# Kernel tuning notes

Hardware: AMD Instinct MI355X
Metric: run time of the kernel (lower is better)

Reference implementation:

```python
import jax, jax.numpy as jnp
import numpy as np

B, T, N = 256, 4096, 64


def setup_inputs() -> dict:
    key = jax.random.key(0)
    u = jax.random.normal(key, (B, T), dtype=jnp.float32)
    # LRU-style stable parameterization: rho chosen so r = exp(-softplus(rho)) = radii
    radii = np.clip(0.9 + 0.0015 * np.arange(N), 1e-6, 1 - 1e-6)
    rho = np.log(np.expm1(-np.log(radii))).astype(np.float32)
    theta = (np.pi * np.arange(N) / N).astype(np.float32)
    return {
        "u": u,
        "rho": jnp.asarray(rho),
        "theta": jnp.asarray(theta),
        "b_real": jnp.ones((N,), jnp.float32),
        "b_imag": jnp.zeros((N,), jnp.float32),
        "c_real": jnp.ones((N,), jnp.float32),
        "c_imag": jnp.zeros((N,), jnp.float32),
    }


def reference(u, rho, theta, b_real, b_imag, c_real, c_imag):
    # lambda = exp(-softplus(rho)) * exp(i*theta), strictly inside unit circle
    r = jnp.exp(-jax.nn.softplus(rho))
    lam = (r.astype(jnp.complex64) * jnp.exp(1j * theta)).astype(jnp.complex64)
    b = (b_real + 1j * b_imag).astype(jnp.complex64)
    c_conj = jnp.conj((c_real + 1j * c_imag).astype(jnp.complex64))
    # precompute driving term b * u_t for all t: (T, B, N)
    bu = jnp.swapaxes(b[None, None, :] * u[:, :, None], 0, 1)

    def step(x, bu_t):
        x = lam * x + bu_t            # (B, N) complex diagonal recurrence
        y_t = jnp.real(x @ c_conj)    # (B,) readout Re(c^H x)
        return x, y_t

    x0 = jnp.zeros((u.shape[0], rho.shape[0]), dtype=jnp.complex64)
    _, ys = jax.lax.scan(step, x0, bu)  # ys: (T, B)
    return jnp.swapaxes(ys, 0, 1)       # (B, T) float32
```

## Files before the change

### kernel.cpp

```cpp
#include <hip/hip_runtime.h>
#include <hip/hip_bf16.h>

#define T_LEN  4096
#define NLAG   5
#define CMAX   575
#define ESTR   728
#define ROUNDS 9

typedef __attribute__((ext_vector_type(8))) short short8;
typedef __attribute__((ext_vector_type(4))) float f32x4;

static __device__ __forceinline__ unsigned short f2bf(float f) {
  __hip_bfloat16 h = __float2bfloat16(f);
  return *reinterpret_cast<unsigned short*>(&h);
}

template <int CTRL>
static __device__ __forceinline__ float dppmov(float x) {
  return __int_as_float(__builtin_amdgcn_update_dpp(
      0, __float_as_int(x), CTRL, 0xF, 0xF, true));
}

#define CVT8(dst, va, vb) {                                                       \
    short8 _v;                                                                    \
    _v[0] = (short)f2bf((va).x); _v[1] = (short)f2bf((va).y);                     \
    _v[2] = (short)f2bf((va).z); _v[3] = (short)f2bf((va).w);                     \
    _v[4] = (short)f2bf((vb).x); _v[5] = (short)f2bf((vb).y);                     \
    _v[6] = (short)f2bf((vb).z); _v[7] = (short)f2bf((vb).w);                     \
    *reinterpret_cast<short8*>(dst) = _v; }

#define LBAR() { asm volatile("s_waitcnt lgkmcnt(0)" ::: "memory");               \
                 __builtin_amdgcn_s_barrier(); }

__global__ __launch_bounds__(512) void ssm_one(
    const float* __restrict__ u, const float* __restrict__ rho,
    const float* __restrict__ theta, const float* __restrict__ br,
    const float* __restrict__ bi, const float* __restrict__ cr,
    const float* __restrict__ ci, float* __restrict__ out) {
  __shared__ __align__(16) unsigned short Ab[2][8192];
  __shared__ __align__(16) unsigned short E8[8 * ESTR];

  const int tid = threadIdx.x;
  const int lane = tid & 63;
  const int w = tid >> 6;
  const bool prod = (w >= 4);
  const int pt = tid & 255;

  const int bid = blockIdx.x;
  const int swz = (bid & 7) * 32 + (bid >> 3);
  const int t0 = (swz & 63) * 64;
  const int b0 = (swz >> 6) * 64;

  const int lrow = lane >> 4, lc16 = lane & 15;
  const float4 z4 = make_float4(0.f, 0.f, 0.f, 0.f);
  float4 av[2][4][2];
  f32x4 acc[2][2] = {};

#define ISSUEA(j, S) { _Pragma("unroll") for (int h_ = 0; h_ < 4; ++h_) {         \
    const int hh = pt + 256 * h_;                                                 \
    const int r_ = hh >> 4, cg = hh & 15;                                         \
    const int gg = t0 - (j) * 128 + cg * 8;                                       \
    if ((unsigned)gg < 4096u) {                                                   \
      const float* p_ = u + (size_t)(b0 + r_) * T_LEN + gg;                       \
      av[S][h_][0] = *reinterpret_cast<const float4*>(p_);                        \
      av[S][h_][1] = *reinterpret_cast<const float4*>(p_ + 4);                    \
    } else { av[S][h_][0] = z4; av[S][h_][1] = z4; } } }

#define WRITEA(buf, S) { _Pragma("unroll") for (int h_ = 0; h_ < 4; ++h_) {       \
    const int hh = pt + 256 * h_;                                                 \
    const int r_ = hh >> 4, cg = hh & 15;                                         \
    const int eo = r_ * 128 + ((cg * 8) ^ ((r_ & 7) << 3));                       \
    CVT8(&Ab[buf][eo], av[S][h_][0], av[S][h_][1]); } }

  if (prod) ISSUEA(0, 0);

  {
    const short8 z8 = {};
    for (int c = tid; c < ESTR; c += 512)
      *reinterpret_cast<short8*>(&E8[c * 8]) = z8;
  }

  const float rh = rho[lane], th = theta[lane];
  const float lr2 = -1.4426950408f * log1pf(expf(rh));
  const float rr_ = exp2f(lr2);
  const float lre = rr_ * __cosf(th), lim = rr_ * __sinf(th);
  const float brv = br[lane], biv = bi[lane];
  const float crv = cr[lane], civ = ci[lane];
  const float wre = crv * brv + civ * biv;
  const float wim = crv * biv - civ * brv;

  float Lr[9], Li[9];
  Lr[0] = 1.f; Li[0] = 0.f;
#pragma unroll
  for (int i = 1; i <= 8; ++i) {
    Lr[i] = Lr[i - 1] * lre - Li[i - 1] * lim;
    Li[i] = Lr[i - 1] * lim + Li[i - 1] * lre;
  }

  const float d0f = (float)(8 * ROUNDS * w);
  const float rd0 = exp2f(d0f * lr2);
  float f0 = d0f * (th * 0.15915494309f);
  f0 -= floorf(f0);
  const float a0 = 6.2831853072f * f0;
  const float c0 = __cosf(a0), s0 = __sinf(a0);
  float gr = rd0 * (wre * c0 - wim * s0);
  float gi = rd0 * (wre * s0 + wim * c0);

  const bool l0 = lane & 1, l1 = lane & 2, l3 = lane & 8;
  const int sig = ((lane & 1) << 2) | (lane & 2) | ((lane >> 3) & 1);
  const int cc  = ((lane >> 2) & 1) | ((lane >> 3) & 2) | ((lane >> 3) & 4);

  LBAR();

  for (int rnd = 0; rnd < ROUNDS; ++rnd) {
    float v[8];
#pragma unroll
    for (int i2 = 0; i2 < 8; ++i2)
      v[i2] = gr * Lr[i2] - gi * Li[i2];
    { const float ngr = gr * Lr[8] - gi * Li[8];
      const float ngi = gr * Li[8] + gi * Lr[8];
      gr = ngr; gi = ngi; }
    float s4[4];
#pragma unroll
    for (int i = 0; i < 4; ++i) {
      const float t = l0 ? v[i + 4] : v[i];
      const float u2 = l0 ? v[i] : v[i + 4];
      s4[i] = t + dppmov<0xB1>(u2);
    }
    float s2[2];
#pragma unroll
    for (int i = 0; i < 2; ++i) {
      const float t = l1 ? s4[i + 2] : s4[i];
      const float u2 = l1 ? s4[i] : s4[i + 2];
      s2[i] = t + dppmov<0x4E>(u2);
    }
    float y;
    { const float t = l3 ? s2[1] : s2[0];
      const float u2 = l3 ? s2[0] : s2[1];
      y = t + dppmov<0x128>(u2); }
    y += __shfl_xor(y, 4);
    y += __shfl_xor(y, 16);
    y += __shfl_xor(y, 32);
    const int d = 72 * w + 8 * rnd + sig;
    const int yy = CMAX - d;
    if (yy >= cc) E8[cc * ESTR + (yy - cc)] = f2bf(y);
  }

  if (prod) { WRITEA(0, 0); ISSUEA(1, 1); }
  LBAR();

#define COMPUTE(jj, buf) {                                                        \
    const unsigned short* A = Ab[buf];                                            \
    const int wm = w >> 1, wn = w & 1;                                            \
    const int pB = 7 - (lc16 & 7);                                                \
    _Pragma("unroll") for (int ks = 0; ks < 4; ++ks) {                            \
      short8 af[2], bfr[2];                                                       \
      _Pragma("unroll") for (int ft = 0; ft < 2; ++ft) {                          \
        const int r = wm * 32 + ft * 16 + lc16;                                   \
        const int pe = (ks * 32 + lrow * 8) ^ ((r & 7) << 3);                     \
        af[ft] = *reinterpret_cast<const short8*>(&A[r * 128 + pe]); }            \
      _Pragma("unroll") for (int fn = 0; fn < 2; ++fn) {                          \
        const int rB = wn * 32 + fn * 16 + lc16;                                  \
        const int x0 = CMAX - (jj) * 128 - rB + ks * 32 + lrow * 8 - pB;          \
        bfr[fn] = *reinterpret_cast<const short8*>(&E8[pB * ESTR + x0]); }        \
      _Pragma("unroll") for (int ft = 0; ft < 2; ++ft)                            \
        _Pragma("unroll") for (int fn = 0; fn < 2; ++fn)                          \
          acc[ft][fn] = __builtin_amdgcn_mfma_f32_16x16x32_bf16(                  \
              af[ft], bfr[fn], acc[ft][fn], 0, 0, 0); } }

#pragma unroll
  for (int j = 0; j < NLAG; ++j) {
    if (prod) {
      if (j + 1 < NLAG) WRITEA((j + 1) & 1, (j + 1) & 1);
      if (j + 2 < NLAG) ISSUEA(j + 2, j & 1);
    } else {
      COMPUTE(j, j & 1);
    }
    if (j < NLAG - 1) LBAR();
  }

  if (!prod) {
    const int wm = w >> 1, wn = w & 1;
#pragma unroll
    for (int ft = 0; ft < 2; ++ft)
#pragma unroll
      for (int fn = 0; fn < 2; ++fn)
#pragma unroll
        for (int rg = 0; rg < 4; ++rg) {
          const int row = b0 + wm * 32 + ft * 16 + lrow * 4 + rg;
          const int col = t0 + wn * 32 + fn * 16 + lc16;
          out[(size_t)row * T_LEN + col] = acc[ft][fn][rg];
        }
  }
#undef ISSUEA
#undef WRITEA
#undef COMPUTE
}

extern "C" void kernel_launch(void* const* d_in, const int* in_sizes, int n_in,
                              void* d_out, int out_size, void* d_ws, size_t ws_size,
                              hipStream_t stream) {
  const float* u     = (const float*)d_in[0];
  const float* rho   = (const float*)d_in[1];
  const float* theta = (const float*)d_in[2];
  const float* br    = (const float*)d_in[3];
  const float* bi    = (const float*)d_in[4];
  const float* cr    = (const float*)d_in[5];
  const float* ci    = (const float*)d_in[6];
  float* out = (float*)d_out;

  ssm_one<<<256, 512, 0, stream>>>(u, rho, theta, br, bi, cr, ci, out);
}
```

Measured before the change: 12.99 us.

## Double block to 1024 threads with split-K consumers and dedicated producer waves

The block grows from 512 to 1024 threads. Eight producer waves now share the global load of the input tile, each doing half as many loads per thread. Eight consumer waves split the MFMA K-loop in half, and the two partial accumulators are summed through a new LDS scratch buffer before the output store. The impulse-response table is now computed only by consumer waves while producers zero the table and issue the first load. This aims to cut per-wave serial work and latency in a short, latency-bound kernel. In exchange it adds a reduction barrier, extra LDS, and tighter register limits from the new launch bounds.

```diff
diff --git a/kernel.cpp b/kernel.cpp
--- a/kernel.cpp
+++ b/kernel.cpp
@@ -32,19 +32,20 @@
 #define LBAR() { asm volatile("s_waitcnt lgkmcnt(0)" ::: "memory");               \
                  __builtin_amdgcn_s_barrier(); }
 
-__global__ __launch_bounds__(512) void ssm_one(
+__global__ __launch_bounds__(1024, 4) void ssm_one(
     const float* __restrict__ u, const float* __restrict__ rho,
     const float* __restrict__ theta, const float* __restrict__ br,
     const float* __restrict__ bi, const float* __restrict__ cr,
     const float* __restrict__ ci, float* __restrict__ out) {
   __shared__ __align__(16) unsigned short Ab[2][8192];
   __shared__ __align__(16) unsigned short E8[8 * ESTR];
+  __shared__ __align__(16) f32x4 scr[16][64];
 
   const int tid = threadIdx.x;
   const int lane = tid & 63;
   const int w = tid >> 6;
-  const bool prod = (w >= 4);
-  const int pt = tid & 255;
+  const bool prod = (w >= 8);
+  const int ptid = tid & 511;
 
   const int bid = blockIdx.x;
   const int swz = (bid & 7) * 32 + (bid >> 3);
@@ -53,11 +54,11 @@
 
   const int lrow = lane >> 4, lc16 = lane & 15;
   const float4 z4 = make_float4(0.f, 0.f, 0.f, 0.f);
-  float4 av[2][4][2];
+  float4 av[2][2][2];
   f32x4 acc[2][2] = {};
 
-#define ISSUEA(j, S) { _Pragma("unroll") for (int h_ = 0; h_ < 4; ++h_) {         \
-    const int hh = pt + 256 * h_;                                                 \
+#define ISSUEA(j, S) { _Pragma("unroll") for (int h_ = 0; h_ < 2; ++h_) {         \
+    const int hh = ptid + 512 * h_;                                               \
     const int r_ = hh >> 4, cg = hh & 15;                                         \
     const int gg = t0 - (j) * 128 + cg * 8;                                       \
     if ((unsigned)gg < 4096u) {                                                   \
@@ -66,102 +67,101 @@
       av[S][h_][1] = *reinterpret_cast<const float4*>(p_ + 4);                    \
     } else { av[S][h_][0] = z4; av[S][h_][1] = z4; } } }
 
-#define WRITEA(buf, S) { _Pragma("unroll") for (int h_ = 0; h_ < 4; ++h_) {       \
-    const int hh = pt + 256 * h_;                                                 \
+#define WRITEA(buf, S) { _Pragma("unroll") for (int h_ = 0; h_ < 2; ++h_) {       \
+    const int hh = ptid + 512 * h_;                                               \
     const int r_ = hh >> 4, cg = hh & 15;                                         \
     const int eo = r_ * 128 + ((cg * 8) ^ ((r_ & 7) << 3));                       \
     CVT8(&Ab[buf][eo], av[S][h_][0], av[S][h_][1]); } }
 
-  if (prod) ISSUEA(0, 0);
-
-  {
-    const short8 z8 = {};
-    for (int c = tid; c < ESTR; c += 512)
-      *reinterpret_cast<short8*>(&E8[c * 8]) = z8;
-  }
-
-  const float rh = rho[lane], th = theta[lane];
-  const float lr2 = -1.4426950408f * log1pf(expf(rh));
-  const float rr_ = exp2f(lr2);
-  const float lre = rr_ * __cosf(th), lim = rr_ * __sinf(th);
-  const float brv = br[lane], biv = bi[lane];
-  const float crv = cr[lane], civ = ci[lane];
-  const float wre = crv * brv + civ * biv;
-  const float wim = crv * biv - civ * brv;
-
-  float Lr[9], Li[9];
-  Lr[0] = 1.f; Li[0] = 0.f;
-#pragma unroll
-  for (int i = 1; i <= 8; ++i) {
-    Lr[i] = Lr[i - 1] * lre - Li[i - 1] * lim;
-    Li[i] = Lr[i - 1] * lim + Li[i - 1] * lre;
-  }
-
-  const float d0f = (float)(8 * ROUNDS * w);
-  const float rd0 = exp2f(d0f * lr2);
-  float f0 = d0f * (th * 0.15915494309f);
-  f0 -= floorf(f0);
-  const float a0 = 6.2831853072f * f0;
-  const float c0 = __cosf(a0), s0 = __sinf(a0);
-  float gr = rd0 * (wre * c0 - wim * s0);
-  float gi = rd0 * (wre * s0 + wim * c0);
-
+  float Lr[9], Li[9], gr = 0.f, gi = 0.f;
   const bool l0 = lane & 1, l1 = lane & 2, l3 = lane & 8;
   const int sig = ((lane & 1) << 2) | (lane & 2) | ((lane >> 3) & 1);
   const int cc  = ((lane >> 2) & 1) | ((lane >> 3) & 2) | ((lane >> 3) & 4);
 
+  if (prod) {
+    ISSUEA(0, 0);
+    const short8 z8 = {};
+    for (int c = ptid; c < ESTR; c += 512)
+      *reinterpret_cast<short8*>(&E8[c * 8]) = z8;
+  } else {
+    const float rh = rho[lane], th = theta[lane];
+    const float lr2 = -1.4426950408f * log1pf(expf(rh));
+    const float rr_ = exp2f(lr2);
+    const float lre = rr_ * __cosf(th), lim = rr_ * __sinf(th);
+    const float brv = br[lane], biv = bi[lane];
+    const float crv = cr[lane], civ = ci[lane];
+    const float wre = crv * brv + civ * biv;
+    const float wim = crv * biv - civ * brv;
+    Lr[0] = 1.f; Li[0] = 0.f;
+#pragma unroll
+    for (int i = 1; i <= 8; ++i) {
+      Lr[i] = Lr[i - 1] * lre - Li[i - 1] * lim;
+      Li[i] = Lr[i - 1] * lim + Li[i - 1] * lre;
+    }
+    const float d0f = (float)(8 * ROUNDS * w);
+    const float rd0 = exp2f(d0f * lr2);
+    float f0 = d0f * (th * 0.15915494309f);
+    f0 -= floorf(f0);
+    const float a0 = 6.2831853072f * f0;
+    const float c0 = __cosf(a0), s0 = __sinf(a0);
+    gr = rd0 * (wre * c0 - wim * s0);
+    gi = rd0 * (wre * s0 + wim * c0);
+  }
+
   LBAR();
 
-  for (int rnd = 0; rnd < ROUNDS; ++rnd) {
-    float v[8];
-#pragma unroll
-    for (int i2 = 0; i2 < 8; ++i2)
-      v[i2] = gr * Lr[i2] - gi * Li[i2];
-    { const float ngr = gr * Lr[8] - gi * Li[8];
-      const float ngi = gr * Li[8] + gi * Lr[8];
-      gr = ngr; gi = ngi; }
-    float s4[4];
-#pragma unroll
-    for (int i = 0; i < 4; ++i) {
-      const float t = l0 ? v[i + 4] : v[i];
-      const float u2 = l0 ? v[i] : v[i + 4];
-      s4[i] = t + dppmov<0xB1>(u2);
-    }
-    float s2[2];
-#pragma unroll
-    for (int i = 0; i < 2; ++i) {
-      const float t = l1 ? s4[i + 2] : s4[i];
-      const float u2 = l1 ? s4[i] : s4[i + 2];
-      s2[i] = t + dppmov<0x4E>(u2);
-    }
-    float y;
-    { const float t = l3 ? s2[1] : s2[0];
-      const float u2 = l3 ? s2[0] : s2[1];
-      y = t + dppmov<0x128>(u2); }
-    y += __shfl_xor(y, 4);
-    y += __shfl_xor(y, 16);
-    y += __shfl_xor(y, 32);
-    const int d = 72 * w + 8 * rnd + sig;
-    const int yy = CMAX - d;
-    if (yy >= cc) E8[cc * ESTR + (yy - cc)] = f2bf(y);
-  }
-
-  if (prod) { WRITEA(0, 0); ISSUEA(1, 1); }
+#define ROUND(rnd) {                                                              \
+    float v[8];                                                                   \
+    _Pragma("unroll") for (int i2 = 0; i2 < 8; ++i2)                              \
+      v[i2] = gr * Lr[i2] - gi * Li[i2];                        \
+    { const float ngr = gr * Lr[8] - gi * Li[8];                                  \
+      const float ngi = gr * Li[8] + gi * Lr[8];                                  \
+      gr = ngr; gi = ngi; }                                                       \
+    float s4[4];                                                                  \
+    _Pragma("unroll") for (int i = 0; i < 4; ++i) {                               \
+      const float t_ = l0 ? v[i + 4] : v[i];                                      \
+      const float u2 = l0 ? v[i] : v[i + 4];                                      \
+      s4[i] = t_ + dppmov<0xB1>(u2); }                                            \
+    float s2[2];                                                                  \
+    _Pragma("unroll") for (int i = 0; i < 2; ++i) {                               \
+      const float t_ = l1 ? s4[i + 2] : s4[i];                                    \
+      const float u2 = l1 ? s4[i] : s4[i + 2];                                    \
+      s2[i] = t_ + dppmov<0x4E>(u2); }                                            \
+    float y_;                                                                     \
+    { const float t_ = l3 ? s2[1] : s2[0];                                        \
+      const float u2 = l3 ? s2[0] : s2[1];                                        \
+      y_ = t_ + dppmov<0x128>(u2); }                                              \
+    y_ += __shfl_xor(y_, 4);                                                      \
+    y_ += __shfl_xor(y_, 16);                                                     \
+    y_ += __shfl_xor(y_, 32);                                                     \
+    const int d_ = 72 * w + 8 * (rnd) + sig;                                      \
+    const int yy = CMAX - d_;                                                     \
+    if (yy >= cc) E8[cc * ESTR + (yy - cc)] = f2bf(y_); }
+
+  if (prod) {
+    WRITEA(0, 0);
+    ISSUEA(1, 1);
+  } else {
+    ROUND(0); ROUND(1); ROUND(2); ROUND(3); ROUND(4);
+    ROUND(5); ROUND(6); ROUND(7); ROUND(8);
+  }
   LBAR();
+
+  const int qr = (w >> 2) & 1, qc = (w >> 1) & 1, kh = w & 1;
 
 #define COMPUTE(jj, buf) {                                                        \
     const unsigned short* A = Ab[buf];                                            \
-    const int wm = w >> 1, wn = w & 1;                                            \
     const int pB = 7 - (lc16 & 7);                                                \
-    _Pragma("unroll") for (int ks = 0; ks < 4; ++ks) {                            \
+    _Pragma("unroll") for (int ksl = 0; ksl < 2; ++ksl) {                         \
+      const int ks = kh * 2 + ksl;                                                \
       short8 af[2], bfr[2];                                                       \
       _Pragma("unroll") for (int ft = 0; ft < 2; ++ft) {                          \
-        const int r = wm * 32 + ft * 16 + lc16;                                   \
+        const int r = qr * 32 + ft * 16 + lc16;                                   \
         const int pe = (ks * 32 + lrow * 8) ^ ((r & 7) << 3);                     \
         af[ft] = *reinterpret_cast<const short8*>(&A[r * 128 + pe]); }            \
       _Pragma("unroll") for (int fn = 0; fn < 2; ++fn) {                          \
-        const int rB = wn * 32 + fn * 16 + lc16;                                  \
-        const int x0 = CMAX - (jj) * 128 - rB + ks * 32 + lrow * 8 - pB;          \
+        const int tc = qc * 32 + fn * 16 + lc16;                                  \
+        const int x0 = CMAX - (jj) * 128 - tc + ks * 32 + lrow * 8 - pB;          \
         bfr[fn] = *reinterpret_cast<const short8*>(&E8[pB * ESTR + x0]); }        \
       _Pragma("unroll") for (int ft = 0; ft < 2; ++ft)                            \
         _Pragma("unroll") for (int fn = 0; fn < 2; ++fn)                          \
@@ -179,22 +179,33 @@
     if (j < NLAG - 1) LBAR();
   }
 
-  if (!prod) {
-    const int wm = w >> 1, wn = w & 1;
+  const int qid = qr * 2 + qc;
+  if (!prod && kh == 1) {
 #pragma unroll
     for (int ft = 0; ft < 2; ++ft)
 #pragma unroll
       for (int fn = 0; fn < 2; ++fn)
+        scr[qid * 4 + ft * 2 + fn][lane] = acc[ft][fn];
+  }
+  LBAR();
+  if (!prod && kh == 0) {
+#pragma unroll
+    for (int ft = 0; ft < 2; ++ft)
+#pragma unroll
+      for (int fn = 0; fn < 2; ++fn) {
+        const f32x4 s = scr[qid * 4 + ft * 2 + fn][lane];
 #pragma unroll
         for (int rg = 0; rg < 4; ++rg) {
-          const int row = b0 + wm * 32 + ft * 16 + lrow * 4 + rg;
-          const int col = t0 + wn * 32 + fn * 16 + lc16;
-          out[(size_t)row * T_LEN + col] = acc[ft][fn][rg];
+          const int row = b0 + qr * 32 + ft * 16 + lrow * 4 + rg;
+          const int col = t0 + qc * 32 + fn * 16 + lc16;
+          out[(size_t)row * T_LEN + col] = acc[ft][fn][rg] + s[rg];
         }
+      }
   }
 #undef ISSUEA
 #undef WRITEA
 #undef COMPUTE
+#undef ROUND
 }
 
 extern "C" void kernel_launch(void* const* d_in, const int* in_sizes, int n_in,
@@ -209,5 +220,5 @@
   const float* ci    = (const float*)d_in[6];
   float* out = (float*)d_out;
 
-  ssm_one<<<256, 512, 0, stream>>>(u, rho, theta, br, bi, cr, ci, out);
-}
+  ssm_one<<<256, 1024, 0, stream>>>(u, rho, theta, br, bi, cr, ci, out);
+}
```

After: 12.24 us. 5.7% less time.
